# Optimization experiments

Measured on AMD Instinct MI355X. Metric: run time of the kernel, lower is better.

Reference implementation:

```python
import jax, jax.numpy as jnp
import numpy as np


def setup_inputs() -> dict:
    key = jax.random.key(0)
    ks = jax.random.split(key, 8)
    B, N, E, F = 8, 200, 128, 16
    scale = 0.05
    return {
        "h": jax.random.normal(ks[0], (B, N, E), dtype=jnp.float32),
        "edge_features": jax.random.normal(ks[1], (B, N, N, F), dtype=jnp.float32),
        "W": jax.random.uniform(ks[2], (B, N, N), dtype=jnp.float32),
        "W_node": jax.random.normal(ks[3], (E, E), dtype=jnp.float32) * scale,
        "W_edge": jax.random.normal(ks[4], (E, F), dtype=jnp.float32) * scale,
        "W_weight": jax.random.normal(ks[5], (E, 1), dtype=jnp.float32) * scale,
        "W_out": jax.random.normal(ks[6], (E, E), dtype=jnp.float32) * scale,
        "b_out": jax.random.normal(ks[7], (E,), dtype=jnp.float32) * scale,
    }


def reference(h, edge_features, W, W_node, W_edge, W_weight, W_out, b_out):
    # hi: [B,N,1,E]  (node_proj)
    hi = jnp.einsum('bne,fe->bnf', h, W_node)[:, :, None, :]
    # ej: [B,N,N,E]  (edge_proj)
    ej = jnp.einsum('bnmf,ef->bnme', edge_features, W_edge)
    # wij: [B,N,N,E] (weight_proj of scalar W)
    wij = W[..., None] * W_weight[:, 0]  # broadcast [B,N,N,1]*[E]
    msg = jnp.tanh(hi + ej + wij)        # [B,N,N,E]
    agg = msg.mean(axis=2)               # [B,N,E]
    return jnp.einsum('bne,fe->bnf', agg, W_out) + b_out
```

## Files before the change

kernel.cpp:

```cpp
#include <hip/hip_runtime.h>

typedef __attribute__((ext_vector_type(4))) float  f32x4;
typedef __attribute__((ext_vector_type(8))) short  short8;
typedef __attribute__((ext_vector_type(2))) unsigned int u32x2;

#define NN 200
#define EDIM 128
#define FDIM 16
#define BN_TOTAL 1600
#define NCHUNK 7

#define WS_WE    0
#define WS_WWT   2048
#define WS_WOUT  2176
#define WSF_HI    10240
#define WSF_PART  215040

__device__ __forceinline__ unsigned short f2bf(float f) {
    unsigned u = __float_as_uint(f);
    u += 0x7FFFu + ((u >> 16) & 1u);
    return (unsigned short)(u >> 16);
}
__device__ __forceinline__ short8 cvt8(f32x4 a, f32x4 b) {
    short8 r;
    r[0]=(short)f2bf(a.x); r[1]=(short)f2bf(a.y); r[2]=(short)f2bf(a.z); r[3]=(short)f2bf(a.w);
    r[4]=(short)f2bf(b.x); r[5]=(short)f2bf(b.y); r[6]=(short)f2bf(b.z); r[7]=(short)f2bf(b.w);
    return r;
}
__device__ __forceinline__ float tanh_fast(float x) {
    float e = __builtin_amdgcn_exp2f(x * 2.8853900817779268f);
    float r = __builtin_amdgcn_rcpf(1.0f + e);
    return __builtin_fmaf(-2.0f, r, 1.0f);
}

__global__ __launch_bounds__(128) void setup_kernel(
    const float* __restrict__ h, const float* __restrict__ W_node,
    const float* __restrict__ W_edge, const float* __restrict__ W_weight,
    const float* __restrict__ W_out, void* __restrict__ wsv)
{
    unsigned short* wsb = (unsigned short*)wsv;
    float* wsf = (float*)wsv;
    const int blk = blockIdx.x;
    const int tid = threadIdx.x;

    if (blk < 100) {
        const int lane = tid & 63;
        const int w    = tid >> 6;
        const int g    = lane >> 4;
        const int l15  = lane & 15;
        const int r0   = blk * 16;

        short8 afr[4];
#pragma unroll
        for (int ks = 0; ks < 4; ++ks) {
            const float* p = h + (size_t)(r0 + l15) * EDIM + ks * 32 + g * 8;
            afr[ks] = cvt8(*(const f32x4*)p, *(const f32x4*)(p + 4));
        }
#pragma unroll
        for (int e2 = 0; e2 < 4; ++e2) {
            const int et = w * 4 + e2;
            f32x4 acc = {0.f, 0.f, 0.f, 0.f};
#pragma unroll
            for (int ks = 0; ks < 4; ++ks) {
                const float* p = W_node + (size_t)(et * 16 + l15) * EDIM + ks * 32 + g * 8;
                short8 bfr = cvt8(*(const f32x4*)p, *(const f32x4*)(p + 4));
                acc = __builtin_amdgcn_mfma_f32_16x16x32_bf16(afr[ks], bfr, acc, 0, 0, 0);
            }
#pragma unroll
            for (int r = 0; r < 4; ++r)
                wsf[WSF_HI + (size_t)(r0 + g * 4 + r) * EDIM + et * 16 + l15] = acc[r];
        }
    } else {
        for (int c = (blk - 100) * 128 + tid; c < 4640; c += 8 * 128) {
            const float* src; unsigned short* dst;
            if (c < 512)      { src = W_edge   + c * 4;         dst = wsb + WS_WE   + c * 4; }
            else if (c < 544) { src = W_weight + (c - 512) * 4; dst = wsb + WS_WWT  + (c - 512) * 4; }
            else              { src = W_out    + (c - 544) * 4; dst = wsb + WS_WOUT + (c - 544) * 4; }
            f32x4 v = *(const f32x4*)src;
            u32x2 pk = { (unsigned)f2bf(v.x) | ((unsigned)f2bf(v.y) << 16),
                         (unsigned)f2bf(v.z) | ((unsigned)f2bf(v.w) << 16) };
            *(u32x2*)dst = pk;
        }
    }
}

__global__ __launch_bounds__(64) void msg_kernel(
    const float* __restrict__ ef, const float* __restrict__ Wadj,
    void* __restrict__ wsv)
{
    const unsigned short* wsb = (const unsigned short*)wsv;
    const float* wsf = (const float*)wsv;
    float* wsp = (float*)wsv;

    const int blk  = blockIdx.x;
    const int bn   = blk / NCHUNK;
    const int cj   = blk - bn * NCHUNK;
    const int lane = threadIdx.x;
    const int g    = lane >> 4;
    const int l15  = lane & 15;
    const int m0   = cj * 32;

    float hi_e[8];
#pragma unroll
    for (int et = 0; et < 8; ++et)
        hi_e[et] = wsf[WSF_HI + (size_t)bn * EDIM + et * 16 + l15];

    short8 bfrag[8];
#pragma unroll
    for (int et = 0; et < 8; ++et) {
        short8 b = {0, 0, 0, 0, 0, 0, 0, 0};
        if (g < 2)       b = *(const short8*)(wsb + WS_WE + (et * 16 + l15) * FDIM + g * 8);
        else if (g == 2) b[0] = (short)wsb[WS_WWT + et * 16 + l15];
        bfrag[et] = b;
    }

    short8 a0 = {0, 0, 0, 0, 0, 0, 0, 0};
    {
        int row = m0 + l15; if (row > NN - 1) row = NN - 1;
        if (g < 2) {
            const float* p = ef + ((size_t)bn * NN + row) * FDIM + g * 8;
            a0 = cvt8(*(const f32x4*)p, *(const f32x4*)(p + 4));
        } else if (g == 2) {
            a0[0] = (short)f2bf(Wadj[bn * NN + row]);
        }
    }
    short8 a1 = {0, 0, 0, 0, 0, 0, 0, 0};
    const bool has1 = (cj < 6);
    if (has1) {
        int row = m0 + 16 + l15;
        if (g < 2) {
            const float* p = ef + ((size_t)bn * NN + row) * FDIM + g * 8;
            a1 = cvt8(*(const f32x4*)p, *(const f32x4*)(p + 4));
        } else if (g == 2) {
            a1[0] = (short)f2bf(Wadj[bn * NN + row]);
        }
    }

    const bool full0 = (cj < 6) | (g < 2);
    float part[8];
#pragma unroll
    for (int et = 0; et < 8; ++et) part[et] = 0.f;

#pragma unroll
    for (int et = 0; et < 8; ++et) {
        f32x4 c0 = {hi_e[et], hi_e[et], hi_e[et], hi_e[et]};
        c0 = __builtin_amdgcn_mfma_f32_16x16x32_bf16(a0, bfrag[et], c0, 0, 0, 0);
        if (full0)
            part[et] += tanh_fast(c0[0]) + tanh_fast(c0[1])
                      + tanh_fast(c0[2]) + tanh_fast(c0[3]);
    }
    if (has1) {
#pragma unroll
        for (int et = 0; et < 8; ++et) {
            f32x4 c1 = {hi_e[et], hi_e[et], hi_e[et], hi_e[et]};
            c1 = __builtin_amdgcn_mfma_f32_16x16x32_bf16(a1, bfrag[et], c1, 0, 0, 0);
            part[et] += tanh_fast(c1[0]) + tanh_fast(c1[1])
                      + tanh_fast(c1[2]) + tanh_fast(c1[3]);
        }
    }

#pragma unroll
    for (int et = 0; et < 8; ++et) {
        float p = part[et];
        p += __shfl_xor(p, 16);
        p += __shfl_xor(p, 32);
        if (g == 0)
            wsp[WSF_PART + ((size_t)cj * BN_TOTAL + bn) * EDIM + et * 16 + l15] = p;
    }
}

__global__ __launch_bounds__(128) void outproj_kernel(
    const void* __restrict__ wsv, const float* __restrict__ b_out,
    float* __restrict__ out)
{
    const unsigned short* wsb = (const unsigned short*)wsv;
    const float* wsf = (const float*)wsv;
    const int tid  = threadIdx.x;
    const int lane = tid & 63;
    const int w    = tid >> 6;
    const int g    = lane >> 4;
    const int l15  = lane & 15;
    const int r0   = blockIdx.x * 16;

    short8 afr[4];
#pragma unroll
    for (int ks = 0; ks < 4; ++ks) {
        const size_t off = (size_t)(r0 + l15) * EDIM + ks * 32 + g * 8;
        f32x4 s0 = {0.f, 0.f, 0.f, 0.f}, s1 = {0.f, 0.f, 0.f, 0.f};
#pragma unroll
        for (int j = 0; j < NCHUNK; ++j) {
            const float* p = wsf + WSF_PART + (size_t)j * (BN_TOTAL * EDIM) + off;
            s0 += *(const f32x4*)p;
            s1 += *(const f32x4*)(p + 4);
        }
        const float sc = 1.0f / (float)NN;
        afr[ks] = cvt8(s0 * sc, s1 * sc);
    }
#pragma unroll
    for (int f2 = 0; f2 < 4; ++f2) {
        const int ft = w * 4 + f2;
        f32x4 acc = {0.f, 0.f, 0.f, 0.f};
#pragma unroll
        for (int ks = 0; ks < 4; ++ks) {
            short8 b = *(const short8*)(wsb + WS_WOUT + (ft * 16 + l15) * EDIM + ks * 32 + g * 8);
            acc = __builtin_amdgcn_mfma_f32_16x16x32_bf16(afr[ks], b, acc, 0, 0, 0);
        }
        const float bo = b_out[ft * 16 + l15];
#pragma unroll
        for (int r = 0; r < 4; ++r)
            out[(size_t)(r0 + g * 4 + r) * EDIM + ft * 16 + l15] = acc[r] + bo;
    }
}

extern "C" void kernel_launch(void* const* d_in, const int* in_sizes, int n_in,
                              void* d_out, int out_size, void* d_ws, size_t ws_size,
                              hipStream_t stream) {
    const float* h        = (const float*)d_in[0];
    const float* ef       = (const float*)d_in[1];
    const float* W        = (const float*)d_in[2];
    const float* W_node   = (const float*)d_in[3];
    const float* W_edge   = (const float*)d_in[4];
    const float* W_weight = (const float*)d_in[5];
    const float* W_out    = (const float*)d_in[6];
    const float* b_out    = (const float*)d_in[7];
    float* out = (float*)d_out;

    setup_kernel<<<108, 128, 0, stream>>>(h, W_node, W_edge, W_weight, W_out, d_ws);
    msg_kernel<<<BN_TOTAL * NCHUNK, 64, 0, stream>>>(ef, W, d_ws);
    outproj_kernel<<<100, 128, 0, stream>>>(d_ws, b_out, out);
}
```

Measured before the change: 36.32 us.

## Fold tanh into sigmoid sum with padding trick and batch items per block

Writes tanh as 1 - 2*sigmoid, folds the 2/ln2 scale into hi and the bf16 edge weights, and turns the mean into 1 - 0.01*sum of reciprocal sigmoids in the output projection. Padded rows get a large bias through an extra MFMA column (0x4980), which drives their term to zero, so the per-row masking goes away. Each msg block now handles four (bn, chunk) items with software-pipelined loads, and conversions use v_cvt_pk_bf16_f32. Setup and outproj grids are doubled to spread the work over more blocks, at the cost of more register pressure and bf16 rounding of the scaled weights.

```diff
diff --git a/kernel.cpp b/kernel.cpp
--- a/kernel.cpp
+++ b/kernel.cpp
@@ -2,6 +2,7 @@
 
 typedef __attribute__((ext_vector_type(4))) float  f32x4;
 typedef __attribute__((ext_vector_type(8))) short  short8;
+typedef __attribute__((ext_vector_type(4))) unsigned int u32x4;
 typedef __attribute__((ext_vector_type(2))) unsigned int u32x2;
 
 #define NN 200
@@ -9,10 +10,10 @@
 #define FDIM 16
 #define BN_TOTAL 1600
 #define NCHUNK 7
-
-#define WS_WE    0
-#define WS_WWT   2048
-#define WS_WOUT  2176
+#define MSG_BLOCKS 2800
+#define LAMBDA 2.8853900817779268f
+
+#define WS_WOUT_S 2176
 #define WSF_HI    10240
 #define WSF_PART  215040
 
@@ -27,28 +28,34 @@
     r[4]=(short)f2bf(b.x); r[5]=(short)f2bf(b.y); r[6]=(short)f2bf(b.z); r[7]=(short)f2bf(b.w);
     return r;
 }
-__device__ __forceinline__ float tanh_fast(float x) {
-    float e = __builtin_amdgcn_exp2f(x * 2.8853900817779268f);
-    float r = __builtin_amdgcn_rcpf(1.0f + e);
-    return __builtin_fmaf(-2.0f, r, 1.0f);
+__device__ __forceinline__ unsigned cvtpk(float lo, float hi) {
+    unsigned r;
+    asm("v_cvt_pk_bf16_f32 %0, %1, %2" : "=v"(r) : "v"(lo), "v"(hi));
+    return r;
+}
+__device__ __forceinline__ float sigr(float x) {
+    return __builtin_amdgcn_rcpf(1.0f + __builtin_amdgcn_exp2f(x));
 }
 
 __global__ __launch_bounds__(128) void setup_kernel(
     const float* __restrict__ h, const float* __restrict__ W_node,
     const float* __restrict__ W_edge, const float* __restrict__ W_weight,
-    const float* __restrict__ W_out, void* __restrict__ wsv)
+    const float* __restrict__ W_out,
+    unsigned short* __restrict__ wcvt,
+    unsigned short* __restrict__ wout,
+    float* __restrict__ hi_arr)
 {
-    unsigned short* wsb = (unsigned short*)wsv;
-    float* wsf = (float*)wsv;
     const int blk = blockIdx.x;
     const int tid = threadIdx.x;
 
-    if (blk < 100) {
+    if (blk < 200) {
+        const int rb   = blk >> 1;
+        const int eh   = blk & 1;
         const int lane = tid & 63;
         const int w    = tid >> 6;
         const int g    = lane >> 4;
         const int l15  = lane & 15;
-        const int r0   = blk * 16;
+        const int r0   = rb * 16;
 
         short8 afr[4];
 #pragma unroll
@@ -57,8 +64,8 @@
             afr[ks] = cvt8(*(const f32x4*)p, *(const f32x4*)(p + 4));
         }
 #pragma unroll
-        for (int e2 = 0; e2 < 4; ++e2) {
-            const int et = w * 4 + e2;
+        for (int e2 = 0; e2 < 2; ++e2) {
+            const int et = eh * 4 + w * 2 + e2;
             f32x4 acc = {0.f, 0.f, 0.f, 0.f};
 #pragma unroll
             for (int ks = 0; ks < 4; ++ks) {
@@ -68,15 +75,16 @@
             }
 #pragma unroll
             for (int r = 0; r < 4; ++r)
-                wsf[WSF_HI + (size_t)(r0 + g * 4 + r) * EDIM + et * 16 + l15] = acc[r];
+                hi_arr[(size_t)(r0 + g * 4 + r) * EDIM + et * 16 + l15] = acc[r] * LAMBDA;
         }
     } else {
-        for (int c = (blk - 100) * 128 + tid; c < 4640; c += 8 * 128) {
-            const float* src; unsigned short* dst;
-            if (c < 512)      { src = W_edge   + c * 4;         dst = wsb + WS_WE   + c * 4; }
-            else if (c < 544) { src = W_weight + (c - 512) * 4; dst = wsb + WS_WWT  + (c - 512) * 4; }
-            else              { src = W_out    + (c - 544) * 4; dst = wsb + WS_WOUT + (c - 544) * 4; }
+        for (int c = (blk - 200) * 128 + tid; c < 4640; c += 8 * 128) {
+            const float* src; unsigned short* dst; float sc;
+            if (c < 512)      { src = W_edge   + c * 4;         dst = wcvt + c * 4;               sc = LAMBDA; }
+            else if (c < 544) { src = W_weight + (c - 512) * 4; dst = wcvt + 2048 + (c - 512) * 4; sc = LAMBDA; }
+            else              { src = W_out    + (c - 544) * 4; dst = wout + (c - 544) * 4;        sc = 1.0f; }
             f32x4 v = *(const f32x4*)src;
+            v.x *= sc; v.y *= sc; v.z *= sc; v.w *= sc;
             u32x2 pk = { (unsigned)f2bf(v.x) | ((unsigned)f2bf(v.y) << 16),
                          (unsigned)f2bf(v.z) | ((unsigned)f2bf(v.w) << 16) };
             *(u32x2*)dst = pk;
@@ -84,103 +92,124 @@
     }
 }
 
+#define LOAD_ITEM(BE, BH, BN, CJ)                                             \
+  do {                                                                        \
+    _Pragma("unroll")                                                         \
+    for (int t_ = 0; t_ < 2; ++t_) {                                          \
+      int row_  = (CJ) * 32 + t_ * 16 + l15;                                  \
+      int rowc_ = row_ > NN - 1 ? NN - 1 : row_;                              \
+      if (g < 2) {                                                            \
+        const float* p_ = ef + ((size_t)(BN) * NN + rowc_) * FDIM + g * 8;    \
+        BE[t_ * 2]     = *(const f32x4*)p_;                                   \
+        BE[t_ * 2 + 1] = *(const f32x4*)(p_ + 4);                             \
+      } else if (g == 2) {                                                    \
+        BE[t_ * 2].x = Wadj[(BN) * NN + rowc_];                               \
+      }                                                                       \
+    }                                                                         \
+    _Pragma("unroll")                                                         \
+    for (int et_ = 0; et_ < 8; ++et_)                                         \
+      BH[et_] = hi_arr[(size_t)(BN) * EDIM + et_ * 16 + l15];                 \
+  } while (0)
+
+#define COMP_ITEM(BE, BH, BN, CJ)                                             \
+  do {                                                                        \
+    float Sr_[8];                                                             \
+    _Pragma("unroll")                                                         \
+    for (int et_ = 0; et_ < 8; ++et_) Sr_[et_] = 0.f;                         \
+    _Pragma("unroll")                                                         \
+    for (int t_ = 0; t_ < 2; ++t_) {                                          \
+      short8 a_;                                                              \
+      if (g < 2) {                                                            \
+        u32x4 pk_ = { cvtpk(BE[t_*2].x,   BE[t_*2].y),                        \
+                      cvtpk(BE[t_*2].z,   BE[t_*2].w),                        \
+                      cvtpk(BE[t_*2+1].x, BE[t_*2+1].y),                      \
+                      cvtpk(BE[t_*2+1].z, BE[t_*2+1].w) };                    \
+        a_ = __builtin_bit_cast(short8, pk_);                                 \
+      } else {                                                                \
+        short8 z_ = {0,0,0,0,0,0,0,0};                                        \
+        if (g == 2) {                                                         \
+          z_[0] = (short)f2bf(BE[t_*2].x);                                    \
+          if ((CJ) * 32 + t_ * 16 + l15 >= NN) z_[1] = (short)0x4980;         \
+        }                                                                     \
+        a_ = z_;                                                              \
+      }                                                                       \
+      _Pragma("unroll")                                                       \
+      for (int et_ = 0; et_ < 8; ++et_) {                                     \
+        f32x4 c_ = {BH[et_], BH[et_], BH[et_], BH[et_]};                      \
+        c_ = __builtin_amdgcn_mfma_f32_16x16x32_bf16(a_, bfrag[et_], c_, 0, 0, 0); \
+        Sr_[et_] += sigr(c_[0]) + sigr(c_[1]) + sigr(c_[2]) + sigr(c_[3]);    \
+      }                                                                       \
+    }                                                                         \
+    _Pragma("unroll")                                                         \
+    for (int et_ = 0; et_ < 8; ++et_) {                                       \
+      float p_ = Sr_[et_];                                                    \
+      p_ += __shfl_xor(p_, 16);                                               \
+      p_ += __shfl_xor(p_, 32);                                               \
+      Sr_[et_] = p_;                                                          \
+    }                                                                         \
+    if (g == 0) {                                                             \
+      float* dst_ = part + ((size_t)(CJ) * BN_TOTAL + (BN)) * EDIM + l15;     \
+      _Pragma("unroll")                                                       \
+      for (int et_ = 0; et_ < 8; ++et_) dst_[et_ * 16] = Sr_[et_];            \
+    }                                                                         \
+  } while (0)
+
 __global__ __launch_bounds__(64) void msg_kernel(
     const float* __restrict__ ef, const float* __restrict__ Wadj,
-    void* __restrict__ wsv)
+    const unsigned short* __restrict__ wcvt,
+    const float* __restrict__ hi_arr,
+    float* __restrict__ part)
 {
-    const unsigned short* wsb = (const unsigned short*)wsv;
-    const float* wsf = (const float*)wsv;
-    float* wsp = (float*)wsv;
-
-    const int blk  = blockIdx.x;
-    const int bn   = blk / NCHUNK;
-    const int cj   = blk - bn * NCHUNK;
     const int lane = threadIdx.x;
     const int g    = lane >> 4;
     const int l15  = lane & 15;
-    const int m0   = cj * 32;
-
-    float hi_e[8];
-#pragma unroll
-    for (int et = 0; et < 8; ++et)
-        hi_e[et] = wsf[WSF_HI + (size_t)bn * EDIM + et * 16 + l15];
 
     short8 bfrag[8];
 #pragma unroll
     for (int et = 0; et < 8; ++et) {
         short8 b = {0, 0, 0, 0, 0, 0, 0, 0};
-        if (g < 2)       b = *(const short8*)(wsb + WS_WE + (et * 16 + l15) * FDIM + g * 8);
-        else if (g == 2) b[0] = (short)wsb[WS_WWT + et * 16 + l15];
+        if (g < 2) b = *(const short8*)(wcvt + (et * 16 + l15) * FDIM + g * 8);
+        else if (g == 2) {
+            b[0] = (short)wcvt[2048 + et * 16 + l15];
+            b[1] = (short)0x4980;
+        }
         bfrag[et] = b;
     }
 
-    short8 a0 = {0, 0, 0, 0, 0, 0, 0, 0};
-    {
-        int row = m0 + l15; if (row > NN - 1) row = NN - 1;
-        if (g < 2) {
-            const float* p = ef + ((size_t)bn * NN + row) * FDIM + g * 8;
-            a0 = cvt8(*(const f32x4*)p, *(const f32x4*)(p + 4));
-        } else if (g == 2) {
-            a0[0] = (short)f2bf(Wadj[bn * NN + row]);
-        }
-    }
-    short8 a1 = {0, 0, 0, 0, 0, 0, 0, 0};
-    const bool has1 = (cj < 6);
-    if (has1) {
-        int row = m0 + 16 + l15;
-        if (g < 2) {
-            const float* p = ef + ((size_t)bn * NN + row) * FDIM + g * 8;
-            a1 = cvt8(*(const f32x4*)p, *(const f32x4*)(p + 4));
-        } else if (g == 2) {
-            a1[0] = (short)f2bf(Wadj[bn * NN + row]);
-        }
-    }
-
-    const bool full0 = (cj < 6) | (g < 2);
-    float part[8];
-#pragma unroll
-    for (int et = 0; et < 8; ++et) part[et] = 0.f;
-
-#pragma unroll
-    for (int et = 0; et < 8; ++et) {
-        f32x4 c0 = {hi_e[et], hi_e[et], hi_e[et], hi_e[et]};
-        c0 = __builtin_amdgcn_mfma_f32_16x16x32_bf16(a0, bfrag[et], c0, 0, 0, 0);
-        if (full0)
-            part[et] += tanh_fast(c0[0]) + tanh_fast(c0[1])
-                      + tanh_fast(c0[2]) + tanh_fast(c0[3]);
-    }
-    if (has1) {
-#pragma unroll
-        for (int et = 0; et < 8; ++et) {
-            f32x4 c1 = {hi_e[et], hi_e[et], hi_e[et], hi_e[et]};
-            c1 = __builtin_amdgcn_mfma_f32_16x16x32_bf16(a1, bfrag[et], c1, 0, 0, 0);
-            part[et] += tanh_fast(c1[0]) + tanh_fast(c1[1])
-                      + tanh_fast(c1[2]) + tanh_fast(c1[3]);
-        }
-    }
-
-#pragma unroll
-    for (int et = 0; et < 8; ++et) {
-        float p = part[et];
-        p += __shfl_xor(p, 16);
-        p += __shfl_xor(p, 32);
-        if (g == 0)
-            wsp[WSF_PART + ((size_t)cj * BN_TOTAL + bn) * EDIM + et * 16 + l15] = p;
-    }
+    const int idx = blockIdx.x * 4;
+    int bn_[4], cj_[4];
+#pragma unroll
+    for (int k = 0; k < 4; ++k) {
+        int id = idx + k;
+        int b  = (id * 18725) >> 17;
+        bn_[k] = b; cj_[k] = id - b * 7;
+    }
+
+    f32x4 beA[4], beB[4];
+    float bhA[8], bhB[8];
+
+    LOAD_ITEM(beA, bhA, bn_[0], cj_[0]);
+    LOAD_ITEM(beB, bhB, bn_[1], cj_[1]);
+    COMP_ITEM(beA, bhA, bn_[0], cj_[0]);
+    LOAD_ITEM(beA, bhA, bn_[2], cj_[2]);
+    COMP_ITEM(beB, bhB, bn_[1], cj_[1]);
+    LOAD_ITEM(beB, bhB, bn_[3], cj_[3]);
+    COMP_ITEM(beA, bhA, bn_[2], cj_[2]);
+    COMP_ITEM(beB, bhB, bn_[3], cj_[3]);
 }
 
 __global__ __launch_bounds__(128) void outproj_kernel(
-    const void* __restrict__ wsv, const float* __restrict__ b_out,
-    float* __restrict__ out)
+    const float* __restrict__ part, const unsigned short* __restrict__ wout,
+    const float* __restrict__ b_out, float* __restrict__ out)
 {
-    const unsigned short* wsb = (const unsigned short*)wsv;
-    const float* wsf = (const float*)wsv;
     const int tid  = threadIdx.x;
     const int lane = tid & 63;
     const int w    = tid >> 6;
     const int g    = lane >> 4;
     const int l15  = lane & 15;
-    const int r0   = blockIdx.x * 16;
+    const int rb   = blockIdx.x >> 1;
+    const int fh   = blockIdx.x & 1;
+    const int r0   = rb * 16;
 
     short8 afr[4];
 #pragma unroll
@@ -189,20 +218,28 @@
         f32x4 s0 = {0.f, 0.f, 0.f, 0.f}, s1 = {0.f, 0.f, 0.f, 0.f};
 #pragma unroll
         for (int j = 0; j < NCHUNK; ++j) {
-            const float* p = wsf + WSF_PART + (size_t)j * (BN_TOTAL * EDIM) + off;
+            const float* p = part + (size_t)j * (BN_TOTAL * EDIM) + off;
             s0 += *(const f32x4*)p;
             s1 += *(const f32x4*)(p + 4);
         }
-        const float sc = 1.0f / (float)NN;
-        afr[ks] = cvt8(s0 * sc, s1 * sc);
-    }
-#pragma unroll
-    for (int f2 = 0; f2 < 4; ++f2) {
-        const int ft = w * 4 + f2;
+        f32x4 a0, a1;
+        a0.x = __builtin_fmaf(-0.01f, s0.x, 1.0f);
+        a0.y = __builtin_fmaf(-0.01f, s0.y, 1.0f);
+        a0.z = __builtin_fmaf(-0.01f, s0.z, 1.0f);
+        a0.w = __builtin_fmaf(-0.01f, s0.w, 1.0f);
+        a1.x = __builtin_fmaf(-0.01f, s1.x, 1.0f);
+        a1.y = __builtin_fmaf(-0.01f, s1.y, 1.0f);
+        a1.z = __builtin_fmaf(-0.01f, s1.z, 1.0f);
+        a1.w = __builtin_fmaf(-0.01f, s1.w, 1.0f);
+        afr[ks] = cvt8(a0, a1);
+    }
+#pragma unroll
+    for (int f2 = 0; f2 < 2; ++f2) {
+        const int ft = fh * 4 + w * 2 + f2;
         f32x4 acc = {0.f, 0.f, 0.f, 0.f};
 #pragma unroll
         for (int ks = 0; ks < 4; ++ks) {
-            short8 b = *(const short8*)(wsb + WS_WOUT + (ft * 16 + l15) * EDIM + ks * 32 + g * 8);
+            short8 b = *(const short8*)(wout + (ft * 16 + l15) * EDIM + ks * 32 + g * 8);
             acc = __builtin_amdgcn_mfma_f32_16x16x32_bf16(afr[ks], b, acc, 0, 0, 0);
         }
         const float bo = b_out[ft * 16 + l15];
@@ -225,7 +262,15 @@
     const float* b_out    = (const float*)d_in[7];
     float* out = (float*)d_out;
 
-    setup_kernel<<<108, 128, 0, stream>>>(h, W_node, W_edge, W_weight, W_out, d_ws);
-    msg_kernel<<<BN_TOTAL * NCHUNK, 64, 0, stream>>>(ef, W, d_ws);
-    outproj_kernel<<<100, 128, 0, stream>>>(d_ws, b_out, out);
-}
+    unsigned short* wsb = (unsigned short*)d_ws;
+    float*          wsf = (float*)d_ws;
+    unsigned short* wcvt   = wsb;
+    unsigned short* wout   = wsb + WS_WOUT_S;
+    float*          hi_arr = wsf + WSF_HI;
+    float*          part   = wsf + WSF_PART;
+
+    setup_kernel<<<208, 128, 0, stream>>>(h, W_node, W_edge, W_weight, W_out,
+                                          wcvt, wout, hi_arr);
+    msg_kernel<<<MSG_BLOCKS, 64, 0, stream>>>(ef, W, wcvt, hi_arr, part);
+    outproj_kernel<<<200, 128, 0, stream>>>(part, wout, b_out, out);
+}
```

Measured after the change: 37.35 us. 2.8% more time.
